# Kernel optimization log

Hardware: AMD Instinct MI355X
Metric: run time of the kernel (lower is better)

The kernel has to match this reference:

```python
import jax, jax.numpy as jnp
import numpy as np

STDDEV = 0.1  # matches Regularizer(stddev=0.1)


def setup_inputs() -> dict:
    key = jax.random.key(0)
    k1, k2, k3, k4 = jax.random.split(key, 4)
    B, S, D = 2048, 256, 128  # batch, num_samples, n_input
    return {
        "x": jax.random.normal(k1, (B, D), dtype=jnp.float32),
        "noise": jax.random.normal(k2, (B, S, D), dtype=jnp.float32),
        "W": jax.random.normal(k3, (D, 1), dtype=jnp.float32) * 0.1,  # inner model weight
        "b": jax.random.normal(k4, (1,), dtype=jnp.float32),          # inner model bias
    }


def reference(x, noise, W, b):
    B, S, D = noise.shape
    # neighborhood: x repeated + Gaussian noise, plus constant column -> [B, S, D+1]
    xl_feat = x[:, None, :] + noise * STDDEV                      # [B, S, D]
    ones = jnp.ones((B, S, 1), dtype=x.dtype)
    xl = jnp.concatenate([xl_feat, ones], axis=-1)                # [B, S, D+1]

    # inner model (linear + sigmoid classifier) evaluated on the neighborhood
    y = jax.nn.sigmoid(xl_feat @ W + b)                           # [B, S, 1]

    # local least-squares fit: Beta = (X^T X)^{-1} X^T y, batched over B
    XtX = jnp.einsum('bsi,bsj->bij', xl, xl)                      # [B, D+1, D+1]
    Xty = jnp.einsum('bsi,bsk->bik', xl, y)                       # [B, D+1, 1]
    Beta = jnp.linalg.solve(XtX, Xty)                             # [B, D+1, 1]

    # linear predictions -> sigmoid -> BCE(target = model output)
    y_lin = jnp.einsum('bsi,bik->bsk', xl, Beta)                  # [B, S, 1]
    logp = jax.nn.log_sigmoid(y_lin)
    log1mp = jax.nn.log_sigmoid(-y_lin)
    bce = -(y * logp + (1.0 - y) * log1mp)                        # [B, S, 1]
    # mean over stacked per-sample BCE means == global mean (equal sizes)
    return jnp.mean(bce)
```

## Files before the change

kernel.cpp:

```cpp
#include <hip/hip_runtime.h>
#include <math.h>

#define NB 2048
#define NS 256
#define ND 128
#define NCOL 129
#define LDA 132
#define TS 32
#define XTP 40
#define BSTRIDE 132
#define STDDEV 0.1f

typedef __attribute__((ext_vector_type(8))) short bf16x8;
typedef __attribute__((ext_vector_type(4))) float f32x4;

__device__ inline unsigned short f32_to_bf16_rn(float f) {
  unsigned int u = __float_as_uint(f);
  unsigned int r = (u + 0x7FFFu + ((u >> 16) & 1u)) >> 16;
  return (unsigned short)r;
}
__device__ inline float bf16u_to_f32(unsigned short h) {
  return __uint_as_float(((unsigned int)h) << 16);
}
__device__ inline float rdlane(float v, int lane) {
// ... 37 lines not shown
  cornb = fmaf(-mb_, bc##c, cornb); \
  cornr = fmaf(-mb_, rh##c, cornr); \
  UPDS }

#define PUBROW(c) \
  *(float4*)&rbp[(c) * LDA + txc0] = make_float4(a##c##_0, a##c##_1, a##c##_2, a##c##_3); \
  *(float4*)&rbp[(c) * LDA + txc1] = make_float4(a##c##_4, a##c##_5, a##c##_6, a##c##_7);

#define TRAIL_C(c) { \
  const float4 o0_ = *(const float4*)&rbp[(c) * LDA + ty8]; \
  const float4 o1_ = *(const float4*)&rbp[(c) * LDA + ty8 + 4]; \
  const float4 c0_ = *(const float4*)&rbp[(c) * LDA + txc0]; \
  const float4 c1_ = *(const float4*)&rbp[(c) * LDA + txc1]; \
  const float pk_ = pd[(c)]; \
  const float m0 = o0_.x*pk_, m1 = o0_.y*pk_, m2 = o0_.z*pk_, m3 = o0_.w*pk_; \
  const float m4 = o1_.x*pk_, m5 = o1_.y*pk_, m6 = o1_.z*pk_, m7 = o1_.w*pk_; \
  const float rc0 = c0_.x, rc1 = c0_.y, rc2 = c0_.z, rc3 = c0_.w; \
  const float rc4 = c1_.x, rc5 = c1_.y, rc6 = c1_.z, rc7 = c1_.w; \
  FOR_ALL(ACC_UPD) \
  hr0 = fmaf(m0, rp[(c)], hr0); hr1 = fmaf(m1, rp[(c)], hr1); \
  hr2 = fmaf(m2, rp[(c)], hr2); hr3 = fmaf(m3, rp[(c)], hr3); \
  hr4 = fmaf(m4, rp[(c)], hr4); hr5 = fmaf(m5, rp[(c)], hr5); \
  hr6 = fmaf(m6, rp[(c)], hr6); hr7 = fmaf(m7, rp[(c)], hr7); \
  hb0 = fmaf(m0, bp[(c)], hb0); hb1 = fmaf(m1, bp[(c)], hb1); \
  hb2 = fmaf(m2, bp[(c)], hb2); hb3 = fmaf(m3, bp[(c)], hb3); \
  hb4 = fmaf(m4, bp[(c)], hb4); hb5 = fmaf(m5, bp[(c)], hb5); \
  hb6 = fmaf(m6, bp[(c)], hb6); hb7 = fmaf(m7, bp[(c)], hb7); }

#define PC_U(cc, J, SRC, bev) { const float u_ = rdlane(a##cc##_##J, SRC); \
  rh##cc = fmaf(-u_, bev, rh##cc); }
#define PC_S(c, UPDS) { be##c = rh##c * pd##c; UPDS }

#define PCT_ROW(i) const float ps##i = hi \
  ? fmaf(a##i##_4, be0, fmaf(a##i##_5, be1, fmaf(a##i##_6, be2, a##i##_7 * be3))) \
  : fmaf(a##i##_0, be0, fmaf(a##i##_1, be1, fmaf(a##i##_2, be2, a##i##_3 * be3)));

#define FOR_J(F) F(0) F(1) F(2) F(3) F(4) F(5) F(6) F(7)
#define CB_DECL(j) f32x4 cb0_##j = {0.f,0.f,0.f,0.f}; f32x4 cb1_##j = {0.f,0.f,0.f,0.f};

#define MF_J(j) { \
  const bf16x8 Bh = *(const bf16x8*)&XTh[(16*(j) + tx)*XTP + kq]; \
  const bf16x8 Bl = *(const bf16x8*)&XTl[(16*(j) + tx)*XTP + kq]; \
  cb0_##j = __builtin_amdgcn_mfma_f32_16x16x32_bf16(Ah0, Bh, cb0_##j, 0,0,0); \
  cb0_##j = __builtin_amdgcn_mfma_f32_16x16x32_bf16(Ah0, Bl, cb0_##j, 0,0,0); \
  cb0_##j = __builtin_amdgcn_mfma_f32_16x16x32_bf16(Al0, Bh, cb0_##j, 0,0,0); \
  cb1_##j = __builtin_amdgcn_mfma_f32_16x16x32_bf16(Ah1, Bh, cb1_##j, 0,0,0); \
  cb1_##j = __builtin_amdgcn_mfma_f32_16x16x32_bf16(Ah1, Bl, cb1_##j, 0,0,0); \
  cb1_##j = __builtin_amdgcn_mfma_f32_16x16x32_bf16(Al1, Bh, cb1_##j, 0,0,0); }

#define TCONV(u, HV, LV, e) { \
  const float xf_ = sA[(sh + (u)) * LDA + d]; \
  const unsigned short hh_ = f32_to_bf16_rn(xf_); \
  const float hf_ = bf16u_to_f32(hh_); \
  const unsigned short ll_ = f32_to_bf16_rn(xf_ - hf_); \
  HV[e] = (short)hh_; LV[e] = (short)ll_; }

#define STAGE_IT(it, nv) { \
  const int idx_ = t + (it) * 256; \
  const int s_ = idx_ >> 5, d4_ = idx_ & 31; \
  const float4 xq_ = *(const float4*)&xv[d4_ * 4]; \
  float4 xl_; \
  xl_.x = xq_.x + STDDEV * nv.x; \
  xl_.y = xq_.y + STDDEV * nv.y; \
  xl_.z = xq_.z + STDDEV * nv.z; \
  xl_.w = xq_.w + STDDEV * nv.w; \
  *(float4*)&sA[s_ * LDA + d4_ * 4] = xl_; }

#define BW_BJ(b, j) \
  myband[(16*(b) + q4 + 0)*132 + 16*(j) + tx] = cb##b##_##j[0]; \
  myband[(16*(b) + q4 + 1)*132 + 16*(j) + tx] = cb##b##_##j[1]; \
  myband[(16*(b) + q4 + 2)*132 + 16*(j) + tx] = cb##b##_##j[2]; \
  myband[(16*(b) + q4 + 3)*132 + 16*(j) + tx] = cb##b##_##j[3];
#define BW_ALL \
  BW_BJ(0,0) BW_BJ(0,1) BW_BJ(0,2) BW_BJ(0,3) BW_BJ(0,4) BW_BJ(0,5) BW_BJ(0,6) BW_BJ(0,7) \
  BW_BJ(1,0) BW_BJ(1,1) BW_BJ(1,2) BW_BJ(1,3) BW_BJ(1,4) BW_BJ(1,5) BW_BJ(1,6) BW_BJ(1,7)
#define BR_ROW(i) { \
  const float4 lo_ = *(const float4*)&myband[(q8 + (i))*132 + txc0]; \
  const float4 hi_ = *(const float4*)&myband[(q8 + (i))*132 + txc1]; \
  a##i##_0 = lo_.x; a##i##_1 = lo_.y; a##i##_2 = lo_.z; a##i##_3 = lo_.w; \
  a##i##_4 = hi_.x; a##i##_5 = hi_.y; a##i##_6 = hi_.z; a##i##_7 = hi_.w; }
#define BR_ALL \
  BR_ROW(0) BR_ROW(1) BR_ROW(2) BR_ROW(3) BR_ROW(4) BR_ROW(5) BR_ROW(6) BR_ROW(7)

__global__ __launch_bounds__(256, 2)
void k_fit(const float* __restrict__ x, const float* __restrict__ noise,
           const float* __restrict__ W, const float* __restrict__ bptr,
           float* __restrict__ Beta) {
  __shared__ __align__(16) float region0[9344];
  __shared__ __align__(16) float pdiag[NCOL + 3];
  __shared__ __align__(16) float bcol[NCOL + 3];
  __shared__ __align__(16) float rhs[NCOL + 3];
  __shared__ __align__(16) float betaL[NCOL + 3];
  __shared__ __align__(16) float yt[TS];
  __shared__ __align__(16) float Wl[128];
  __shared__ __align__(16) float xv[128];

  float* sA = region0;
  unsigned short* XTh = (unsigned short*)(region0 + 4224);
  unsigned short* XTl = (unsigned short*)(region0 + 4224 + 2560);
  float* band = region0;
  float* rbuf = region0;
  float* sp0  = region0 + 2112;
  float* sp1  = region0 + 2240;

  const int t  = threadIdx.x;
  const int b  = blockIdx.x;
  const int tx = t & 15;
  const int ty = t >> 4;
  const int wv = t >> 6;
  const int txc0 = tx * 4;
  const int txc1 = 64 + tx * 4;
  const int ty8 = ty * 8;
  const int q4 = 4 * (ty & 3);
  const int q8 = 8 * (ty & 3);
  const int kq = 8 * (ty & 3);
  const float bscal = bptr[0];

  if (t < 128) { Wl[t] = W[t]; xv[t] = x[(size_t)b * ND + t]; }

  FOR_J(CB_DECL)
  float col_acc = 0.f, xty_acc = 0.f;

  const float* nbase = noise + (size_t)b * (NS * ND);

  float4 nv0, nv1, nv2, nv3;
  {
    const float4* src = (const float4*)nbase;
    nv0 = src[t]; nv1 = src[t + 256]; nv2 = src[t + 512]; nv3 = src[t + 768];
  }

  for (int s0 = 0; s0 < NS; s0 += TS) {
    __syncthreads();
    {
      STAGE_IT(0, nv0) STAGE_IT(1, nv1) STAGE_IT(2, nv2) STAGE_IT(3, nv3)
      if (t < TS) sA[t * LDA + ND] = 1.0f;
    }
    if (s0 + TS < NS) {
      const float4* src = (const float4*)(nbase + (size_t)(s0 + TS) * ND);
      nv0 = src[t]; nv1 = src[t + 256]; nv2 = src[t + 512]; nv3 = src[t + 768];
    }
    __syncthreads();
    {
      const int d = t >> 1;
      const int sh = (t & 1) * 16;
      bf16x8 h0, h1, l0, l1;
      TCONV(0,h0,l0,0) TCONV(1,h0,l0,1) TCONV(2,h0,l0,2) TCONV(3,h0,l0,3)
      TCONV(4,h0,l0,4) TCONV(5,h0,l0,5) TCONV(6,h0,l0,6) TCONV(7,h0,l0,7)
      TCONV(8,h1,l1,0) TCONV(9,h1,l1,1) TCONV(10,h1,l1,2) TCONV(11,h1,l1,3)
      TCONV(12,h1,l1,4) TCONV(13,h1,l1,5) TCONV(14,h1,l1,6) TCONV(15,h1,l1,7)
      *(bf16x8*)&XTh[d * XTP + sh]     = h0;
      *(bf16x8*)&XTh[d * XTP + sh + 8] = h1;
      *(bf16x8*)&XTl[d * XTP + sh]     = l0;
      *(bf16x8*)&XTl[d * XTP + sh + 8] = l1;
    }
    {
      int sl = t >> 3, p = t & 7;
      float acw = 0.f;
#pragma unroll
      for (int d = 0; d < 4; ++d) {
        float4 a = *(const float4*)&sA[sl * LDA + p * 16 + d * 4];
        float4 w = *(const float4*)&Wl[p * 16 + d * 4];
        acw += a.x * w.x + a.y * w.y + a.z * w.z + a.w * w.w;
      }
      acw += __shfl_xor(acw, 1);
      acw += __shfl_xor(acw, 2);
      acw += __shfl_xor(acw, 4);
      if (p == 0) yt[sl] = 1.f / (1.f + expf(-(acw + bscal)));
    }
    __syncthreads();
    if (t < NCOL) {
      for (int s = 0; s < TS; ++s) {
        float v = sA[s * LDA + t];
        col_acc += v;
        xty_acc += yt[s] * v;
      }
    }
    {
      const bf16x8 Ah0 = *(const bf16x8*)&XTh[(32*wv + tx)*XTP + kq];
      const bf16x8 Al0 = *(const bf16x8*)&XTl[(32*wv + tx)*XTP + kq];
      const bf16x8 Ah1 = *(const bf16x8*)&XTh[(32*wv + 16 + tx)*XTP + kq];
      const bf16x8 Al1 = *(const bf16x8*)&XTl[(32*wv + 16 + tx)*XTP + kq];
      MF_J(0) MF_J(1) MF_J(2) MF_J(3) MF_J(4) MF_J(5) MF_J(6) MF_J(7)
    }
  }
  if (t < NCOL) { bcol[t] = col_acc; rhs[t] = xty_acc; }
  __syncthreads();

  FOR_ALL(ACC_DECL)
  {
    float* myband = band + (wv & 1) * 4224;
    if (wv < 2) {
      BW_ALL
      asm volatile("s_waitcnt lgkmcnt(0)" ::: "memory");
      BR_ALL
      asm volatile("s_waitcnt lgkmcnt(0)" ::: "memory");
    }
    __syncthreads();
    if (wv >= 2) {
      BW_ALL
      asm volatile("s_waitcnt lgkmcnt(0)" ::: "memory");
      BR_ALL
      asm volatile("s_waitcnt lgkmcnt(0)" ::: "memory");
    }
    __syncthreads();
  }

#pragma unroll 1
  for (int p = 0; p < 16; ++p) {
    const int p8 = p * 8;
    const int ol = (p < 8) ? (p << 1) : ((p - 8) << 1);
    float* rbp = &rbuf[(p & 1) * (8 * LDA)];
    if (ty == p) {
      asm volatile("s_waitcnt lgkmcnt(0)" ::: "memory");
      const float4 rq0 = *(const float4*)&rhs[p8];
      const float4 rq1 = *(const float4*)&rhs[p8 + 4];
      const float4 bq0 = *(const float4*)&bcol[p8];
      const float4 bq1 = *(const float4*)&bcol[p8 + 4];
      float rh0 = rq0.x, rh1 = rq0.y, rh2 = rq0.z, rh3 = rq0.w;
      float rh4 = rq1.x, rh5 = rq1.y, rh6 = rq1.z, rh7 = rq1.w;
      float bc0 = bq0.x, bc1 = bq0.y, bc2 = bq0.z, bc3 = bq0.w;
      float bc4 = bq1.x, bc5 = bq1.y, bc6 = bq1.z, bc7 = bq1.w;
      float cornr = rhs[ND], cornb = bcol[ND];
      const int lsrc0 = ((p & 3) << 4) + ol;
      const int lsrc1 = lsrc0 + 1;
      if (p < 8) {
        PF_STEP(0, 0,1,2,3, PF_U(0,1) PF_U(0,2) PF_U(0,3) PF_U(0,4) PF_U(0,5) PF_U(0,6) PF_U(0,7))
        PF_STEP(1, 0,1,2,3, PF_U(1,2) PF_U(1,3) PF_U(1,4) PF_U(1,5) PF_U(1,6) PF_U(1,7))
        PF_STEP(2, 0,1,2,3, PF_U(2,3) PF_U(2,4) PF_U(2,5) PF_U(2,6) PF_U(2,7))
        PF_STEP(3, 0,1,2,3, PF_U(3,4) PF_U(3,5) PF_U(3,6) PF_U(3,7))
        PF_STEP(4, 0,1,2,3, PF_U(4,5) PF_U(4,6) PF_U(4,7))
        PF_STEP(5, 0,1,2,3, PF_U(5,6) PF_U(5,7))
        PF_STEP(6, 0,1,2,3, PF_U(6,7))
        PF_STEP(7, 0,1,2,3, )
      } else {
        PF_STEP(0, 4,5,6,7, PF_U(0,1) PF_U(0,2) PF_U(0,3) PF_U(0,4) PF_U(0,5) PF_U(0,6) PF_U(0,7))
        PF_STEP(1, 4,5,6,7, PF_U(1,2) PF_U(1,3) PF_U(1,4) PF_U(1,5) PF_U(1,6) PF_U(1,7))
        PF_STEP(2, 4,5,6,7, PF_U(2,3) PF_U(2,4) PF_U(2,5) PF_U(2,6) PF_U(2,7))
        PF_STEP(3, 4,5,6,7, PF_U(3,4) PF_U(3,5) PF_U(3,6) PF_U(3,7))
        PF_STEP(4, 4,5,6,7, PF_U(4,5) PF_U(4,6) PF_U(4,7))
        PF_STEP(5, 4,5,6,7, PF_U(5,6) PF_U(5,7))
        PF_STEP(6, 4,5,6,7, PF_U(6,7))
        PF_STEP(7, 4,5,6,7, )
      }
      PUBROW(0) PUBROW(1) PUBROW(2) PUBROW(3)
      PUBROW(4) PUBROW(5) PUBROW(6) PUBROW(7)
      if (tx == 0) {
        *(float4*)&rhs[p8]     = make_float4(rh0, rh1, rh2, rh3);
        *(float4*)&rhs[p8 + 4] = make_float4(rh4, rh5, rh6, rh7);
      }
      if (tx == 1) {
        *(float4*)&bcol[p8]     = make_float4(bc0, bc1, bc2, bc3);
        *(float4*)&bcol[p8 + 4] = make_float4(bc4, bc5, bc6, bc7);
      }
      if (tx == 2) { rhs[ND] = cornr; bcol[ND] = cornb; }
    }
    __syncthreads();
    if (ty > p) {
      const float4 d0_ = *(const float4*)&pdiag[p8];
      const float4 d1_ = *(const float4*)&pdiag[p8 + 4];
      const float4 rq0_ = *(const float4*)&rhs[p8];
      const float4 rq1_ = *(const float4*)&rhs[p8 + 4];
      const float4 bq0_ = *(const float4*)&bcol[p8];
      const float4 bq1_ = *(const float4*)&bcol[p8 + 4];
      const float pd[8] = {d0_.x, d0_.y, d0_.z, d0_.w, d1_.x, d1_.y, d1_.z, d1_.w};
      const float rp[8] = {rq0_.x, rq0_.y, rq0_.z, rq0_.w, rq1_.x, rq1_.y, rq1_.z, rq1_.w};
      const float bp[8] = {bq0_.x, bq0_.y, bq0_.z, bq0_.w, bq1_.x, bq1_.y, bq1_.z, bq1_.w};
      float hr0 = 0.f, hr1 = 0.f, hr2 = 0.f, hr3 = 0.f;
      float hr4 = 0.f, hr5 = 0.f, hr6 = 0.f, hr7 = 0.f;
      float hb0 = 0.f, hb1 = 0.f, hb2 = 0.f, hb3 = 0.f;
      float hb4 = 0.f, hb5 = 0.f, hb6 = 0.f, hb7 = 0.f;
      TRAIL_C(0) TRAIL_C(1) TRAIL_C(2) TRAIL_C(3)
      TRAIL_C(4) TRAIL_C(5) TRAIL_C(6) TRAIL_C(7)
      if (tx == 0) {
        float4 h0 = *(float4*)&rhs[ty8]; float4 h1 = *(float4*)&rhs[ty8 + 4];
        h0.x -= hr0; h0.y -= hr1; h0.z -= hr2; h0.w -= hr3;
        h1.x -= hr4; h1.y -= hr5; h1.z -= hr6; h1.w -= hr7;
        *(float4*)&rhs[ty8] = h0; *(float4*)&rhs[ty8 + 4] = h1;
      }
      if (tx == 1) {
        float4 h0 = *(float4*)&bcol[ty8]; float4 h1 = *(float4*)&bcol[ty8 + 4];
        h0.x -= hb0; h0.y -= hb1; h0.z -= hb2; h0.w -= hb3;
        h1.x -= hb4; h1.y -= hb5; h1.z -= hb6; h1.w -= hb7;
        *(float4*)&bcol[ty8] = h0; *(float4*)&bcol[ty8 + 4] = h1;
      }
    }
  }
  __syncthreads();

  if (t == 0) betaL[ND] = rhs[ND] / bcol[ND];
  if (t < ND) { sp0[t] = 0.f; sp1[t] = 0.f; }
  __syncthreads();
  if (t < ND) rhs[t] = fmaf(-bcol[t], betaL[ND], rhs[t]);
  __syncthreads();
#pragma unroll 1
  for (int p = 15; p >= 0; --p) {
    const int p8 = p * 8;
    const bool hi = (p >= 8);
    const int ol = hi ? ((p - 8) << 1) : (p << 1);
    const int txo0 = ol, txo1 = ol + 1;
    if (ty == p) {
      asm volatile("s_waitcnt lgkmcnt(0)" ::: "memory");
      const float4 rq0 = *(const float4*)&rhs[p8];
      const float4 rq1 = *(const float4*)&rhs[p8 + 4];
      const float4 sq0 = *(const float4*)&sp0[p8];
      const float4 sq1 = *(const float4*)&sp0[p8 + 4];
      const float4 uq0 = *(const float4*)&sp1[p8];
      const float4 uq1 = *(const float4*)&sp1[p8 + 4];
      const float4 dq0 = *(const float4*)&pdiag[p8];
      const float4 dq1 = *(const float4*)&pdiag[p8 + 4];
      float rh0 = rq0.x - sq0.x - uq0.x, rh1 = rq0.y - sq0.y - uq0.y;
      float rh2 = rq0.z - sq0.z - uq0.z, rh3 = rq0.w - sq0.w - uq0.w;
      float rh4 = rq1.x - sq1.x - uq1.x, rh5 = rq1.y - sq1.y - uq1.y;
      float rh6 = rq1.z - sq1.z - uq1.z, rh7 = rq1.w - sq1.w - uq1.w;
      const float pd0 = dq0.x, pd1 = dq0.y, pd2 = dq0.z, pd3 = dq0.w;
      const float pd4 = dq1.x, pd5 = dq1.y, pd6 = dq1.z, pd7 = dq1.w;
      const int lsrc0 = ((p & 3) << 4) + ol;
      const int lsrc1 = lsrc0 + 1;
      float be0, be1, be2, be3, be4, be5, be6, be7;
      if (p < 8) {
        PC_S(7, PC_U(0,3,lsrc1,be7) PC_U(1,3,lsrc1,be7) PC_U(2,3,lsrc1,be7) PC_U(3,3,lsrc1,be7) PC_U(4,3,lsrc1,be7) PC_U(5,3,lsrc1,be7) PC_U(6,3,lsrc1,be7))
        PC_S(6, PC_U(0,2,lsrc1,be6) PC_U(1,2,lsrc1,be6) PC_U(2,2,lsrc1,be6) PC_U(3,2,lsrc1,be6) PC_U(4,2,lsrc1,be6) PC_U(5,2,lsrc1,be6))
        PC_S(5, PC_U(0,1,lsrc1,be5) PC_U(1,1,lsrc1,be5) PC_U(2,1,lsrc1,be5) PC_U(3,1,lsrc1,be5) PC_U(4,1,lsrc1,be5))
        PC_S(4, PC_U(0,0,lsrc1,be4) PC_U(1,0,lsrc1,be4) PC_U(2,0,lsrc1,be4) PC_U(3,0,lsrc1,be4))
        PC_S(3, PC_U(0,3,lsrc0,be3) PC_U(1,3,lsrc0,be3) PC_U(2,3,lsrc0,be3))
        PC_S(2, PC_U(0,2,lsrc0,be2) PC_U(1,2,lsrc0,be2))
        PC_S(1, PC_U(0,1,lsrc0,be1))
        PC_S(0, )
      } else {
        PC_S(7, PC_U(0,7,lsrc1,be7) PC_U(1,7,lsrc1,be7) PC_U(2,7,lsrc1,be7) PC_U(3,7,lsrc1,be7) PC_U(4,7,lsrc1,be7) PC_U(5,7,lsrc1,be7) PC_U(6,7,lsrc1,be7))
        PC_S(6, PC_U(0,6,lsrc1,be6) PC_U(1,6,lsrc1,be6) PC_U(2,6,lsrc1,be6) PC_U(3,6,lsrc1,be6) PC_U(4,6,lsrc1,be6) PC_U(5,6,lsrc1,be6))
        PC_S(5, PC_U(0,5,lsrc1,be5) PC_U(1,5,lsrc1,be5) PC_U(2,5,lsrc1,be5) PC_U(3,5,lsrc1,be5) PC_U(4,5,lsrc1,be5))
        PC_S(4, PC_U(0,4,lsrc1,be4) PC_U(1,4,lsrc1,be4) PC_U(2,4,lsrc1,be4) PC_U(3,4,lsrc1,be4))
        PC_S(3, PC_U(0,7,lsrc0,be3) PC_U(1,7,lsrc0,be3) PC_U(2,7,lsrc0,be3))
        PC_S(2, PC_U(0,6,lsrc0,be2) PC_U(1,6,lsrc0,be2))
        PC_S(1, PC_U(0,5,lsrc0,be1))
        PC_S(0, )
      }
      if (tx == 0) {
        *(float4*)&betaL[p8]     = make_float4(be0, be1, be2, be3);
        *(float4*)&betaL[p8 + 4] = make_float4(be4, be5, be6, be7);
      }
    }
    __syncthreads();
    if (ty < p && (tx == txo0 || tx == txo1)) {
      const bool second = (tx == txo1);
      const float4 beq = *(const float4*)&betaL[p8 + (second ? 4 : 0)];
      float* spd = second ? sp1 : sp0;
      const float be0 = beq.x, be1 = beq.y, be2 = beq.z, be3 = beq.w;
      PCT_ROW(0) PCT_ROW(1) PCT_ROW(2) PCT_ROW(3)
      PCT_ROW(4) PCT_ROW(5) PCT_ROW(6) PCT_ROW(7)
      float4 h0 = *(float4*)&spd[ty8]; float4 h1 = *(float4*)&spd[ty8 + 4];
      h0.x += ps0; h0.y += ps1; h0.z += ps2; h0.w += ps3;
      h1.x += ps4; h1.y += ps5; h1.z += ps6; h1.w += ps7;
      *(float4*)&spd[ty8] = h0; *(float4*)&spd[ty8 + 4] = h1;
    }
    __syncthreads();
  }
  if (t < NCOL) Beta[(size_t)b * BSTRIDE + t] = betaL[t];
}

__device__ inline float logsig(float v) {
  if (v >= 0.f) return -log1pf(expf(-v));
  return v - log1pf(expf(v));
}

__global__ __launch_bounds__(256)
void k_bce(const float* __restrict__ x, const float* __restrict__ noise,
           const float* __restrict__ W, const float* __restrict__ bptr,
           const float* __restrict__ Beta, float* __restrict__ partial) {
  const int t    = threadIdx.x;
  const int lane = t & 31;
  const int grp  = t >> 5;
  const int bb   = blockIdx.x >> 2;
  const size_t sbase = (size_t)blockIdx.x * 64;
  __shared__ float saw[64], sab[64];

  const float4 w4 = *((const float4*)W + lane);
  const float4 x4 = *((const float4*)x + (size_t)bb * 32 + lane);
  const float4 p4 = *((const float4*)(Beta + (size_t)bb * BSTRIDE) + lane);

  for (int it = 0; it < 8; ++it) {
    const size_t idx = sbase + grp * 8 + it;
    float4 n4 = *((const float4*)noise + idx * 32 + lane);
    float4 xl;
    xl.x = x4.x + STDDEV * n4.x;
    xl.y = x4.y + STDDEV * n4.y;
    xl.z = x4.z + STDDEV * n4.z;
    xl.w = x4.w + STDDEV * n4.w;
    float aw = xl.x * w4.x + xl.y * w4.y + xl.z * w4.z + xl.w * w4.w;
    float ab = xl.x * p4.x + xl.y * p4.y + xl.z * p4.z + xl.w * p4.w;
#pragma unroll
    for (int off = 16; off >= 1; off >>= 1) {
      aw += __shfl_xor(aw, off);
      ab += __shfl_xor(ab, off);
    }
    if (lane == 0) { saw[grp * 8 + it] = aw; sab[grp * 8 + it] = ab; }
  }
  __syncthreads();
  if (t < 64) {
    const float bscal = bptr[0];
    const float beta128 = Beta[(size_t)bb * BSTRIDE + 128];
    const float y    = 1.f / (1.f + expf(-(saw[t] + bscal)));
    const float ylin = sab[t] + beta128;
    float v = -(y * logsig(ylin) + (1.f - y) * logsig(-ylin));
#pragma unroll
    for (int off = 32; off >= 1; off >>= 1) v += __shfl_xor(v, off);
    if (t == 0) partial[blockIdx.x] = v;
  }
}

__global__ void k_final(const float* __restrict__ partial, float* __restrict__ out,
                        int n, float inv) {
  __shared__ float red[256];
  float s = 0.f;
  for (int i = threadIdx.x; i < n; i += 256) s += partial[i];
  red[threadIdx.x] = s;
  __syncthreads();
  for (int k = 128; k > 0; k >>= 1) {
    if (threadIdx.x < k) red[threadIdx.x] += red[threadIdx.x + k];
    __syncthreads();
  }
  if (threadIdx.x == 0) out[0] = red[0] * inv;
}

extern "C" void kernel_launch(void* const* d_in, const int* in_sizes, int n_in,
                              void* d_out, int out_size, void* d_ws, size_t ws_size,
                              hipStream_t stream) {
  const float* x     = (const float*)d_in[0];
  const float* noise = (const float*)d_in[1];
  const float* W     = (const float*)d_in[2];
  const float* bptr  = (const float*)d_in[3];
  float* out = (float*)d_out;

  float* Beta = (float*)d_ws;
  const size_t beta_bytes = (size_t)NB * BSTRIDE * sizeof(float);
  float* partial = (float*)((char*)d_ws + ((beta_bytes + 255) & ~(size_t)255));

  const int nblk2 = (NB * NS) / 64;

  k_fit<<<NB, 256, 0, stream>>>(x, noise, W, bptr, Beta);
  k_bce<<<nblk2, 256, 0, stream>>>(x, noise, W, bptr, Beta, partial);
  k_final<<<1, 256, 0, stream>>>(partial, out, nblk2, 1.0f / (float)(NB * NS));
}
```

Measured before the change: 388.3 us.

## Split fused fit kernel into form and solve kernels via global XtX buffer

The monolithic per-batch fit kernel is split into k_form, which accumulates XtX with MFMA and writes it plus column sums and Xty to global workspace, and k_solve, which reloads them and runs the blocked elimination and back-substitution. Each kernel asks for 3 blocks per CU instead of 2, so the memory-bound formation phase and the sync-heavy solve phase no longer share one resource footprint. The cost is an extra round trip of about 128 MB for the XtX matrices through global memory and one more launch. The old fused kernel stays as a fallback when the workspace is too small.

```diff
diff --git a/kernel.cpp b/kernel.cpp
--- a/kernel.cpp
+++ b/kernel.cpp
@@ -143,15 +143,238 @@
 #define BR_ALL \
   BR_ROW(0) BR_ROW(1) BR_ROW(2) BR_ROW(3) BR_ROW(4) BR_ROW(5) BR_ROW(6) BR_ROW(7)
 
-__global__ __launch_bounds__(256, 2)
-void k_fit(const float* __restrict__ x, const float* __restrict__ noise,
-           const float* __restrict__ W, const float* __restrict__ bptr,
-           float* __restrict__ Beta) {
+#define PHASE_A_BODY \
+  for (int s0 = 0; s0 < NS; s0 += TS) { \
+    __syncthreads(); \
+    { STAGE_IT(0, nv0) STAGE_IT(1, nv1) STAGE_IT(2, nv2) STAGE_IT(3, nv3) \
+      if (t < TS) sA[t * LDA + ND] = 1.0f; } \
+    if (s0 + TS < NS) { \
+      const float4* src = (const float4*)(nbase + (size_t)(s0 + TS) * ND); \
+      nv0 = src[t]; nv1 = src[t + 256]; nv2 = src[t + 512]; nv3 = src[t + 768]; \
+    } \
+    __syncthreads(); \
+    { const int d = t >> 1; \
+      const int sh = (t & 1) * 16; \
+      bf16x8 h0, h1, l0, l1; \
+      TCONV(0,h0,l0,0) TCONV(1,h0,l0,1) TCONV(2,h0,l0,2) TCONV(3,h0,l0,3) \
+      TCONV(4,h0,l0,4) TCONV(5,h0,l0,5) TCONV(6,h0,l0,6) TCONV(7,h0,l0,7) \
+      TCONV(8,h1,l1,0) TCONV(9,h1,l1,1) TCONV(10,h1,l1,2) TCONV(11,h1,l1,3) \
+      TCONV(12,h1,l1,4) TCONV(13,h1,l1,5) TCONV(14,h1,l1,6) TCONV(15,h1,l1,7) \
+      *(bf16x8*)&XTh[d * XTP + sh]     = h0; \
+      *(bf16x8*)&XTh[d * XTP + sh + 8] = h1; \
+      *(bf16x8*)&XTl[d * XTP + sh]     = l0; \
+      *(bf16x8*)&XTl[d * XTP + sh + 8] = l1; } \
+    { int sl = t >> 3, p = t & 7; \
+      float acw = 0.f; \
+      _Pragma("unroll") \
+      for (int d = 0; d < 4; ++d) { \
+        float4 a = *(const float4*)&sA[sl * LDA + p * 16 + d * 4]; \
+        float4 w = *(const float4*)&Wl[p * 16 + d * 4]; \
+        acw += a.x * w.x + a.y * w.y + a.z * w.z + a.w * w.w; \
+      } \
+      acw += __shfl_xor(acw, 1); \
+      acw += __shfl_xor(acw, 2); \
+      acw += __shfl_xor(acw, 4); \
+      if (p == 0) yt[sl] = 1.f / (1.f + expf(-(acw + bscal))); } \
+    __syncthreads(); \
+    if (t < NCOL) { \
+      for (int s = 0; s < TS; ++s) { \
+        float v = sA[s * LDA + t]; \
+        col_acc += v; \
+        xty_acc += yt[s] * v; \
+      } } \
+    { const bf16x8 Ah0 = *(const bf16x8*)&XTh[(32*wv + tx)*XTP + kq]; \
+      const bf16x8 Al0 = *(const bf16x8*)&XTl[(32*wv + tx)*XTP + kq]; \
+      const bf16x8 Ah1 = *(const bf16x8*)&XTh[(32*wv + 16 + tx)*XTP + kq]; \
+      const bf16x8 Al1 = *(const bf16x8*)&XTl[(32*wv + 16 + tx)*XTP + kq]; \
+      MF_J(0) MF_J(1) MF_J(2) MF_J(3) MF_J(4) MF_J(5) MF_J(6) MF_J(7) } \
+  }
+
+#define BRIDGE_BODY \
+  { float* myband = band + (wv & 1) * 4224; \
+    if (wv < 2) { \
+      BW_ALL \
+      asm volatile("s_waitcnt lgkmcnt(0)" ::: "memory"); \
+      BR_ALL \
+      asm volatile("s_waitcnt lgkmcnt(0)" ::: "memory"); \
+    } \
+    __syncthreads(); \
+    if (wv >= 2) { \
+      BW_ALL \
+      asm volatile("s_waitcnt lgkmcnt(0)" ::: "memory"); \
+      BR_ALL \
+      asm volatile("s_waitcnt lgkmcnt(0)" ::: "memory"); \
+    } \
+    __syncthreads(); }
+
+#define PHASE_B_BODY \
+  _Pragma("unroll 1") \
+  for (int p = 0; p < 16; ++p) { \
+    const int p8 = p * 8; \
+    const int ol = (p < 8) ? (p << 1) : ((p - 8) << 1); \
+    float* rbp = &rbuf[(p & 1) * (8 * LDA)]; \
+    if (ty == p) { \
+      asm volatile("s_waitcnt lgkmcnt(0)" ::: "memory"); \
+      const float4 rq0 = *(const float4*)&rhs[p8]; \
+      const float4 rq1 = *(const float4*)&rhs[p8 + 4]; \
+      const float4 bq0 = *(const float4*)&bcol[p8]; \
+      const float4 bq1 = *(const float4*)&bcol[p8 + 4]; \
+      float rh0 = rq0.x, rh1 = rq0.y, rh2 = rq0.z, rh3 = rq0.w; \
+      float rh4 = rq1.x, rh5 = rq1.y, rh6 = rq1.z, rh7 = rq1.w; \
+      float bc0 = bq0.x, bc1 = bq0.y, bc2 = bq0.z, bc3 = bq0.w; \
+      float bc4 = bq1.x, bc5 = bq1.y, bc6 = bq1.z, bc7 = bq1.w; \
+      float cornr = rhs[ND], cornb = bcol[ND]; \
+      const int lsrc0 = ((p & 3) << 4) + ol; \
+      const int lsrc1 = lsrc0 + 1; \
+      if (p < 8) { \
+        PF_STEP(0, 0,1,2,3, PF_U(0,1) PF_U(0,2) PF_U(0,3) PF_U(0,4) PF_U(0,5) PF_U(0,6) PF_U(0,7)) \
+        PF_STEP(1, 0,1,2,3, PF_U(1,2) PF_U(1,3) PF_U(1,4) PF_U(1,5) PF_U(1,6) PF_U(1,7)) \
+        PF_STEP(2, 0,1,2,3, PF_U(2,3) PF_U(2,4) PF_U(2,5) PF_U(2,6) PF_U(2,7)) \
+        PF_STEP(3, 0,1,2,3, PF_U(3,4) PF_U(3,5) PF_U(3,6) PF_U(3,7)) \
+        PF_STEP(4, 0,1,2,3, PF_U(4,5) PF_U(4,6) PF_U(4,7)) \
+        PF_STEP(5, 0,1,2,3, PF_U(5,6) PF_U(5,7)) \
+        PF_STEP(6, 0,1,2,3, PF_U(6,7)) \
+        PF_STEP(7, 0,1,2,3, ) \
+      } else { \
+        PF_STEP(0, 4,5,6,7, PF_U(0,1) PF_U(0,2) PF_U(0,3) PF_U(0,4) PF_U(0,5) PF_U(0,6) PF_U(0,7)) \
+        PF_STEP(1, 4,5,6,7, PF_U(1,2) PF_U(1,3) PF_U(1,4) PF_U(1,5) PF_U(1,6) PF_U(1,7)) \
+        PF_STEP(2, 4,5,6,7, PF_U(2,3) PF_U(2,4) PF_U(2,5) PF_U(2,6) PF_U(2,7)) \
+        PF_STEP(3, 4,5,6,7, PF_U(3,4) PF_U(3,5) PF_U(3,6) PF_U(3,7)) \
+        PF_STEP(4, 4,5,6,7, PF_U(4,5) PF_U(4,6) PF_U(4,7)) \
+        PF_STEP(5, 4,5,6,7, PF_U(5,6) PF_U(5,7)) \
+        PF_STEP(6, 4,5,6,7, PF_U(6,7)) \
+        PF_STEP(7, 4,5,6,7, ) \
+      } \
+      PUBROW(0) PUBROW(1) PUBROW(2) PUBROW(3) \
+      PUBROW(4) PUBROW(5) PUBROW(6) PUBROW(7) \
+      if (tx == 0) { \
+        *(float4*)&rhs[p8]     = make_float4(rh0, rh1, rh2, rh3); \
+        *(float4*)&rhs[p8 + 4] = make_float4(rh4, rh5, rh6, rh7); \
+      } \
+      if (tx == 1) { \
+        *(float4*)&bcol[p8]     = make_float4(bc0, bc1, bc2, bc3); \
+        *(float4*)&bcol[p8 + 4] = make_float4(bc4, bc5, bc6, bc7); \
+      } \
+      if (tx == 2) { rhs[ND] = cornr; bcol[ND] = cornb; } \
+    } \
+    __syncthreads(); \
+    if (ty > p) { \
+      const float4 d0_ = *(const float4*)&pdiag[p8]; \
+      const float4 d1_ = *(const float4*)&pdiag[p8 + 4]; \
+      const float4 rq0_ = *(const float4*)&rhs[p8]; \
+      const float4 rq1_ = *(const float4*)&rhs[p8 + 4]; \
+      const float4 bq0_ = *(const float4*)&bcol[p8]; \
+      const float4 bq1_ = *(const float4*)&bcol[p8 + 4]; \
+      const float pd[8] = {d0_.x, d0_.y, d0_.z, d0_.w, d1_.x, d1_.y, d1_.z, d1_.w}; \
+      const float rp[8] = {rq0_.x, rq0_.y, rq0_.z, rq0_.w, rq1_.x, rq1_.y, rq1_.z, rq1_.w}; \
+      const float bp[8] = {bq0_.x, bq0_.y, bq0_.z, bq0_.w, bq1_.x, bq1_.y, bq1_.z, bq1_.w}; \
+      float hr0 = 0.f, hr1 = 0.f, hr2 = 0.f, hr3 = 0.f; \
+      float hr4 = 0.f, hr5 = 0.f, hr6 = 0.f, hr7 = 0.f; \
+      float hb0 = 0.f, hb1 = 0.f, hb2 = 0.f, hb3 = 0.f; \
+      float hb4 = 0.f, hb5 = 0.f, hb6 = 0.f, hb7 = 0.f; \
+      TRAIL_C(0) TRAIL_C(1) TRAIL_C(2) TRAIL_C(3) \
+      TRAIL_C(4) TRAIL_C(5) TRAIL_C(6) TRAIL_C(7) \
+      if (tx == 0) { \
+        float4 h0 = *(float4*)&rhs[ty8]; float4 h1 = *(float4*)&rhs[ty8 + 4]; \
+        h0.x -= hr0; h0.y -= hr1; h0.z -= hr2; h0.w -= hr3; \
+        h1.x -= hr4; h1.y -= hr5; h1.z -= hr6; h1.w -= hr7; \
+        *(float4*)&rhs[ty8] = h0; *(float4*)&rhs[ty8 + 4] = h1; \
+      } \
+      if (tx == 1) { \
+        float4 h0 = *(float4*)&bcol[ty8]; float4 h1 = *(float4*)&bcol[ty8 + 4]; \
+        h0.x -= hb0; h0.y -= hb1; h0.z -= hb2; h0.w -= hb3; \
+        h1.x -= hb4; h1.y -= hb5; h1.z -= hb6; h1.w -= hb7; \
+        *(float4*)&bcol[ty8] = h0; *(float4*)&bcol[ty8 + 4] = h1; \
+      } \
+    } \
+  } \
+  __syncthreads();
+
+#define PHASE_C_BODY \
+  if (t == 0) betaL[ND] = rhs[ND] / bcol[ND]; \
+  if (t < ND) { sp0[t] = 0.f; sp1[t] = 0.f; } \
+  __syncthreads(); \
+  if (t < ND) rhs[t] = fmaf(-bcol[t], betaL[ND], rhs[t]); \
+  __syncthreads(); \
+  _Pragma("unroll 1") \
+  for (int p = 15; p >= 0; --p) { \
+    const int p8 = p * 8; \
+    const bool hi = (p >= 8); \
+    const int ol = hi ? ((p - 8) << 1) : (p << 1); \
+    const int txo0 = ol, txo1 = ol + 1; \
+    if (ty == p) { \
+      asm volatile("s_waitcnt lgkmcnt(0)" ::: "memory"); \
+      const float4 rq0 = *(const float4*)&rhs[p8]; \
+      const float4 rq1 = *(const float4*)&rhs[p8 + 4]; \
+      const float4 sq0 = *(const float4*)&sp0[p8]; \
+      const float4 sq1 = *(const float4*)&sp0[p8 + 4]; \
+      const float4 uq0 = *(const float4*)&sp1[p8]; \
+      const float4 uq1 = *(const float4*)&sp1[p8 + 4]; \
+      const float4 dq0 = *(const float4*)&pdiag[p8]; \
+      const float4 dq1 = *(const float4*)&pdiag[p8 + 4]; \
+      float rh0 = rq0.x - sq0.x - uq0.x, rh1 = rq0.y - sq0.y - uq0.y; \
+      float rh2 = rq0.z - sq0.z - uq0.z, rh3 = rq0.w - sq0.w - uq0.w; \
+      float rh4 = rq1.x - sq1.x - uq1.x, rh5 = rq1.y - sq1.y - uq1.y; \
+      float rh6 = rq1.z - sq1.z - uq1.z, rh7 = rq1.w - sq1.w - uq1.w; \
+      const float pd0 = dq0.x, pd1 = dq0.y, pd2 = dq0.z, pd3 = dq0.w; \
+      const float pd4 = dq1.x, pd5 = dq1.y, pd6 = dq1.z, pd7 = dq1.w; \
+      const int lsrc0 = ((p & 3) << 4) + ol; \
+      const int lsrc1 = lsrc0 + 1; \
+      float be0, be1, be2, be3, be4, be5, be6, be7; \
+      if (p < 8) { \
+        PC_S(7, PC_U(0,3,lsrc1,be7) PC_U(1,3,lsrc1,be7) PC_U(2,3,lsrc1,be7) PC_U(3,3,lsrc1,be7) PC_U(4,3,lsrc1,be7) PC_U(5,3,lsrc1,be7) PC_U(6,3,lsrc1,be7)) \
+        PC_S(6, PC_U(0,2,lsrc1,be6) PC_U(1,2,lsrc1,be6) PC_U(2,2,lsrc1,be6) PC_U(3,2,lsrc1,be6) PC_U(4,2,lsrc1,be6) PC_U(5,2,lsrc1,be6)) \
+        PC_S(5, PC_U(0,1,lsrc1,be5) PC_U(1,1,lsrc1,be5) PC_U(2,1,lsrc1,be5) PC_U(3,1,lsrc1,be5) PC_U(4,1,lsrc1,be5)) \
+        PC_S(4, PC_U(0,0,lsrc1,be4) PC_U(1,0,lsrc1,be4) PC_U(2,0,lsrc1,be4) PC_U(3,0,lsrc1,be4)) \
+        PC_S(3, PC_U(0,3,lsrc0,be3) PC_U(1,3,lsrc0,be3) PC_U(2,3,lsrc0,be3)) \
+        PC_S(2, PC_U(0,2,lsrc0,be2) PC_U(1,2,lsrc0,be2)) \
+        PC_S(1, PC_U(0,1,lsrc0,be1)) \
+        PC_S(0, ) \
+      } else { \
+        PC_S(7, PC_U(0,7,lsrc1,be7) PC_U(1,7,lsrc1,be7) PC_U(2,7,lsrc1,be7) PC_U(3,7,lsrc1,be7) PC_U(4,7,lsrc1,be7) PC_U(5,7,lsrc1,be7) PC_U(6,7,lsrc1,be7)) \
+        PC_S(6, PC_U(0,6,lsrc1,be6) PC_U(1,6,lsrc1,be6) PC_U(2,6,lsrc1,be6) PC_U(3,6,lsrc1,be6) PC_U(4,6,lsrc1,be6) PC_U(5,6,lsrc1,be6)) \
+        PC_S(5, PC_U(0,5,lsrc1,be5) PC_U(1,5,lsrc1,be5) PC_U(2,5,lsrc1,be5) PC_U(3,5,lsrc1,be5) PC_U(4,5,lsrc1,be5)) \
+        PC_S(4, PC_U(0,4,lsrc1,be4) PC_U(1,4,lsrc1,be4) PC_U(2,4,lsrc1,be4) PC_U(3,4,lsrc1,be4)) \
+        PC_S(3, PC_U(0,7,lsrc0,be3) PC_U(1,7,lsrc0,be3) PC_U(2,7,lsrc0,be3)) \
+        PC_S(2, PC_U(0,6,lsrc0,be2) PC_U(1,6,lsrc0,be2)) \
+        PC_S(1, PC_U(0,5,lsrc0,be1)) \
+        PC_S(0, ) \
+      } \
+      if (tx == 0) { \
+        *(float4*)&betaL[p8]     = make_float4(be0, be1, be2, be3); \
+        *(float4*)&betaL[p8 + 4] = make_float4(be4, be5, be6, be7); \
+      } \
+    } \
+    __syncthreads(); \
+    if (ty < p && (tx == txo0 || tx == txo1)) { \
+      const bool second = (tx == txo1); \
+      const float4 beq = *(const float4*)&betaL[p8 + (second ? 4 : 0)]; \
+      float* spd = second ? sp1 : sp0; \
+      const float be0 = beq.x, be1 = beq.y, be2 = beq.z, be3 = beq.w; \
+      PCT_ROW(0) PCT_ROW(1) PCT_ROW(2) PCT_ROW(3) \
+      PCT_ROW(4) PCT_ROW(5) PCT_ROW(6) PCT_ROW(7) \
+      float4 h0 = *(float4*)&spd[ty8]; float4 h1 = *(float4*)&spd[ty8 + 4]; \
+      h0.x += ps0; h0.y += ps1; h0.z += ps2; h0.w += ps3; \
+      h1.x += ps4; h1.y += ps5; h1.z += ps6; h1.w += ps7; \
+      *(float4*)&spd[ty8] = h0; *(float4*)&spd[ty8 + 4] = h1; \
+    } \
+    __syncthreads(); \
+  }
+
+#define ST_ROW(i) { \
+  *(float4*)&Xg[(ty8 + (i))*128 + txc0] = make_float4(a##i##_0, a##i##_1, a##i##_2, a##i##_3); \
+  *(float4*)&Xg[(ty8 + (i))*128 + txc1] = make_float4(a##i##_4, a##i##_5, a##i##_6, a##i##_7); }
+#define LD_ROW(i) { \
+  const float4 lo_ = *(const float4*)&Xg[(ty8 + (i))*128 + txc0]; \
+  const float4 hi_ = *(const float4*)&Xg[(ty8 + (i))*128 + txc1]; \
+  a##i##_0 = lo_.x; a##i##_1 = lo_.y; a##i##_2 = lo_.z; a##i##_3 = lo_.w; \
+  a##i##_4 = hi_.x; a##i##_5 = hi_.y; a##i##_6 = hi_.z; a##i##_7 = hi_.w; }
+
+__global__ __launch_bounds__(256, 3)
+void k_form(const float* __restrict__ x, const float* __restrict__ noise,
+            const float* __restrict__ W, const float* __restrict__ bptr,
+            float* __restrict__ brg, float* __restrict__ xtx) {
   __shared__ __align__(16) float region0[9344];
-  __shared__ __align__(16) float pdiag[NCOL + 3];
-  __shared__ __align__(16) float bcol[NCOL + 3];
-  __shared__ __align__(16) float rhs[NCOL + 3];
-  __shared__ __align__(16) float betaL[NCOL + 3];
   __shared__ __align__(16) float yt[TS];
   __shared__ __align__(16) float Wl[128];
   __shared__ __align__(16) float xv[128];
@@ -160,9 +383,6 @@
   unsigned short* XTh = (unsigned short*)(region0 + 4224);
   unsigned short* XTl = (unsigned short*)(region0 + 4224 + 2560);
   float* band = region0;
-  float* rbuf = region0;
-  float* sp0  = region0 + 2112;
-  float* sp1  = region0 + 2240;
 
   const int t  = threadIdx.x;
   const int b  = blockIdx.x;
@@ -183,240 +403,120 @@
   float col_acc = 0.f, xty_acc = 0.f;
 
   const float* nbase = noise + (size_t)b * (NS * ND);
-
   float4 nv0, nv1, nv2, nv3;
   {
     const float4* src = (const float4*)nbase;
     nv0 = src[t]; nv1 = src[t + 256]; nv2 = src[t + 512]; nv3 = src[t + 768];
   }
 
-  for (int s0 = 0; s0 < NS; s0 += TS) {
-    __syncthreads();
-    {
-      STAGE_IT(0, nv0) STAGE_IT(1, nv1) STAGE_IT(2, nv2) STAGE_IT(3, nv3)
-      if (t < TS) sA[t * LDA + ND] = 1.0f;
-    }
-    if (s0 + TS < NS) {
-      const float4* src = (const float4*)(nbase + (size_t)(s0 + TS) * ND);
-      nv0 = src[t]; nv1 = src[t + 256]; nv2 = src[t + 512]; nv3 = src[t + 768];
-    }
-    __syncthreads();
-    {
-      const int d = t >> 1;
-      const int sh = (t & 1) * 16;
-      bf16x8 h0, h1, l0, l1;
-      TCONV(0,h0,l0,0) TCONV(1,h0,l0,1) TCONV(2,h0,l0,2) TCONV(3,h0,l0,3)
-      TCONV(4,h0,l0,4) TCONV(5,h0,l0,5) TCONV(6,h0,l0,6) TCONV(7,h0,l0,7)
-      TCONV(8,h1,l1,0) TCONV(9,h1,l1,1) TCONV(10,h1,l1,2) TCONV(11,h1,l1,3)
-      TCONV(12,h1,l1,4) TCONV(13,h1,l1,5) TCONV(14,h1,l1,6) TCONV(15,h1,l1,7)
-      *(bf16x8*)&XTh[d * XTP + sh]     = h0;
-      *(bf16x8*)&XTh[d * XTP + sh + 8] = h1;
-      *(bf16x8*)&XTl[d * XTP + sh]     = l0;
-      *(bf16x8*)&XTl[d * XTP + sh + 8] = l1;
-    }
-    {
-      int sl = t >> 3, p = t & 7;
-      float acw = 0.f;
-#pragma unroll
-      for (int d = 0; d < 4; ++d) {
-        float4 a = *(const float4*)&sA[sl * LDA + p * 16 + d * 4];
-        float4 w = *(const float4*)&Wl[p * 16 + d * 4];
-        acw += a.x * w.x + a.y * w.y + a.z * w.z + a.w * w.w;
-      }
-      acw += __shfl_xor(acw, 1);
-      acw += __shfl_xor(acw, 2);
-      acw += __shfl_xor(acw, 4);
-      if (p == 0) yt[sl] = 1.f / (1.f + expf(-(acw + bscal)));
-    }
-    __syncthreads();
-    if (t < NCOL) {
-      for (int s = 0; s < TS; ++s) {
-        float v = sA[s * LDA + t];
-        col_acc += v;
-        xty_acc += yt[s] * v;
-      }
-    }
-    {
-      const bf16x8 Ah0 = *(const bf16x8*)&XTh[(32*wv + tx)*XTP + kq];
-      const bf16x8 Al0 = *(const bf16x8*)&XTl[(32*wv + tx)*XTP + kq];
-      const bf16x8 Ah1 = *(const bf16x8*)&XTh[(32*wv + 16 + tx)*XTP + kq];
-      const bf16x8 Al1 = *(const bf16x8*)&XTl[(32*wv + 16 + tx)*XTP + kq];
-      MF_J(0) MF_J(1) MF_J(2) MF_J(3) MF_J(4) MF_J(5) MF_J(6) MF_J(7)
-    }
-  }
+  PHASE_A_BODY
+
+  if (t < NCOL) {
+    float* br = brg + (size_t)b * 264;
+    br[t] = col_acc; br[132 + t] = xty_acc;
+  }
+  __syncthreads();
+
+  FOR_ALL(ACC_DECL)
+  BRIDGE_BODY
+
+  float* Xg = xtx + (size_t)b * 16384;
+  ST_ROW(0) ST_ROW(1) ST_ROW(2) ST_ROW(3)
+  ST_ROW(4) ST_ROW(5) ST_ROW(6) ST_ROW(7)
+}
+
+__global__ __launch_bounds__(256, 3)
+void k_solve(const float* __restrict__ brg, const float* __restrict__ xtx,
+             float* __restrict__ Beta) {
+  __shared__ __align__(16) float rbuf[2 * 8 * LDA];
+  __shared__ __align__(16) float pdiag[NCOL + 3];
+  __shared__ __align__(16) float bcol[NCOL + 3];
+  __shared__ __align__(16) float rhs[NCOL + 3];
+  __shared__ __align__(16) float betaL[NCOL + 3];
+  __shared__ __align__(16) float sp0[ND], sp1[ND];
+
+  const int t  = threadIdx.x;
+  const int b  = blockIdx.x;
+  const int tx = t & 15;
+  const int ty = t >> 4;
+  const int txc0 = tx * 4;
+  const int txc1 = 64 + tx * 4;
+  const int ty8 = ty * 8;
+
+  FOR_ALL(ACC_DECL)
+  {
+    const float* Xg = xtx + (size_t)b * 16384;
+    LD_ROW(0) LD_ROW(1) LD_ROW(2) LD_ROW(3)
+    LD_ROW(4) LD_ROW(5) LD_ROW(6) LD_ROW(7)
+  }
+  if (t < NCOL) {
+    const float* br = brg + (size_t)b * 264;
+    bcol[t] = br[t]; rhs[t] = br[132 + t];
+  }
+  __syncthreads();
+
+  PHASE_B_BODY
+  PHASE_C_BODY
+
+  if (t < NCOL) Beta[(size_t)b * BSTRIDE + t] = betaL[t];
+}
+
+__global__ __launch_bounds__(256, 2)
+void k_fit_mono(const float* __restrict__ x, const float* __restrict__ noise,
+                const float* __restrict__ W, const float* __restrict__ bptr,
+                float* __restrict__ Beta) {
+  __shared__ __align__(16) float region0[9344];
+  __shared__ __align__(16) float pdiag[NCOL + 3];
+  __shared__ __align__(16) float bcol[NCOL + 3];
+  __shared__ __align__(16) float rhs[NCOL + 3];
+  __shared__ __align__(16) float betaL[NCOL + 3];
+  __shared__ __align__(16) float yt[TS];
+  __shared__ __align__(16) float Wl[128];
+  __shared__ __align__(16) float xv[128];
+
+  float* sA = region0;
+  unsigned short* XTh = (unsigned short*)(region0 + 4224);
+  unsigned short* XTl = (unsigned short*)(region0 + 4224 + 2560);
+  float* band = region0;
+  float* rbuf = region0;
+  float* sp0  = region0 + 2112;
+  float* sp1  = region0 + 2240;
+
+  const int t  = threadIdx.x;
+  const int b  = blockIdx.x;
+  const int tx = t & 15;
+  const int ty = t >> 4;
+  const int wv = t >> 6;
+  const int txc0 = tx * 4;
+  const int txc1 = 64 + tx * 4;
+  const int ty8 = ty * 8;
+  const int q4 = 4 * (ty & 3);
+  const int q8 = 8 * (ty & 3);
+  const int kq = 8 * (ty & 3);
+  const float bscal = bptr[0];
+
+  if (t < 128) { Wl[t] = W[t]; xv[t] = x[(size_t)b * ND + t]; }
+
+  FOR_J(CB_DECL)
+  float col_acc = 0.f, xty_acc = 0.f;
+
+  const float* nbase = noise + (size_t)b * (NS * ND);
+  float4 nv0, nv1, nv2, nv3;
+  {
+    const float4* src = (const float4*)nbase;
+    nv0 = src[t]; nv1 = src[t + 256]; nv2 = src[t + 512]; nv3 = src[t + 768];
+  }
+
+  PHASE_A_BODY
+
   if (t < NCOL) { bcol[t] = col_acc; rhs[t] = xty_acc; }
   __syncthreads();
 
   FOR_ALL(ACC_DECL)
-  {
-    float* myband = band + (wv & 1) * 4224;
-    if (wv < 2) {
-      BW_ALL
-      asm volatile("s_waitcnt lgkmcnt(0)" ::: "memory");
-      BR_ALL
-      asm volatile("s_waitcnt lgkmcnt(0)" ::: "memory");
-    }
-    __syncthreads();
-    if (wv >= 2) {
-      BW_ALL
-      asm volatile("s_waitcnt lgkmcnt(0)" ::: "memory");
-      BR_ALL
-      asm volatile("s_waitcnt lgkmcnt(0)" ::: "memory");
-    }
-    __syncthreads();
-  }
-
-#pragma unroll 1
-  for (int p = 0; p < 16; ++p) {
-    const int p8 = p * 8;
-    const int ol = (p < 8) ? (p << 1) : ((p - 8) << 1);
-    float* rbp = &rbuf[(p & 1) * (8 * LDA)];
-    if (ty == p) {
-      asm volatile("s_waitcnt lgkmcnt(0)" ::: "memory");
-      const float4 rq0 = *(const float4*)&rhs[p8];
-      const float4 rq1 = *(const float4*)&rhs[p8 + 4];
-      const float4 bq0 = *(const float4*)&bcol[p8];
-      const float4 bq1 = *(const float4*)&bcol[p8 + 4];
-      float rh0 = rq0.x, rh1 = rq0.y, rh2 = rq0.z, rh3 = rq0.w;
-      float rh4 = rq1.x, rh5 = rq1.y, rh6 = rq1.z, rh7 = rq1.w;
-      float bc0 = bq0.x, bc1 = bq0.y, bc2 = bq0.z, bc3 = bq0.w;
-      float bc4 = bq1.x, bc5 = bq1.y, bc6 = bq1.z, bc7 = bq1.w;
-      float cornr = rhs[ND], cornb = bcol[ND];
-      const int lsrc0 = ((p & 3) << 4) + ol;
-      const int lsrc1 = lsrc0 + 1;
-      if (p < 8) {
-        PF_STEP(0, 0,1,2,3, PF_U(0,1) PF_U(0,2) PF_U(0,3) PF_U(0,4) PF_U(0,5) PF_U(0,6) PF_U(0,7))
-        PF_STEP(1, 0,1,2,3, PF_U(1,2) PF_U(1,3) PF_U(1,4) PF_U(1,5) PF_U(1,6) PF_U(1,7))
-        PF_STEP(2, 0,1,2,3, PF_U(2,3) PF_U(2,4) PF_U(2,5) PF_U(2,6) PF_U(2,7))
-        PF_STEP(3, 0,1,2,3, PF_U(3,4) PF_U(3,5) PF_U(3,6) PF_U(3,7))
-        PF_STEP(4, 0,1,2,3, PF_U(4,5) PF_U(4,6) PF_U(4,7))
-        PF_STEP(5, 0,1,2,3, PF_U(5,6) PF_U(5,7))
-        PF_STEP(6, 0,1,2,3, PF_U(6,7))
-        PF_STEP(7, 0,1,2,3, )
-      } else {
-        PF_STEP(0, 4,5,6,7, PF_U(0,1) PF_U(0,2) PF_U(0,3) PF_U(0,4) PF_U(0,5) PF_U(0,6) PF_U(0,7))
-        PF_STEP(1, 4,5,6,7, PF_U(1,2) PF_U(1,3) PF_U(1,4) PF_U(1,5) PF_U(1,6) PF_U(1,7))
-        PF_STEP(2, 4,5,6,7, PF_U(2,3) PF_U(2,4) PF_U(2,5) PF_U(2,6) PF_U(2,7))
-        PF_STEP(3, 4,5,6,7, PF_U(3,4) PF_U(3,5) PF_U(3,6) PF_U(3,7))
-        PF_STEP(4, 4,5,6,7, PF_U(4,5) PF_U(4,6) PF_U(4,7))
-        PF_STEP(5, 4,5,6,7, PF_U(5,6) PF_U(5,7))
-        PF_STEP(6, 4,5,6,7, PF_U(6,7))
-        PF_STEP(7, 4,5,6,7, )
-      }
-      PUBROW(0) PUBROW(1) PUBROW(2) PUBROW(3)
-      PUBROW(4) PUBROW(5) PUBROW(6) PUBROW(7)
-      if (tx == 0) {
-        *(float4*)&rhs[p8]     = make_float4(rh0, rh1, rh2, rh3);
-        *(float4*)&rhs[p8 + 4] = make_float4(rh4, rh5, rh6, rh7);
-      }
-      if (tx == 1) {
-        *(float4*)&bcol[p8]     = make_float4(bc0, bc1, bc2, bc3);
-        *(float4*)&bcol[p8 + 4] = make_float4(bc4, bc5, bc6, bc7);
-      }
-      if (tx == 2) { rhs[ND] = cornr; bcol[ND] = cornb; }
-    }
-    __syncthreads();
-    if (ty > p) {
-      const float4 d0_ = *(const float4*)&pdiag[p8];
-      const float4 d1_ = *(const float4*)&pdiag[p8 + 4];
-      const float4 rq0_ = *(const float4*)&rhs[p8];
-      const float4 rq1_ = *(const float4*)&rhs[p8 + 4];
-      const float4 bq0_ = *(const float4*)&bcol[p8];
-      const float4 bq1_ = *(const float4*)&bcol[p8 + 4];
-      const float pd[8] = {d0_.x, d0_.y, d0_.z, d0_.w, d1_.x, d1_.y, d1_.z, d1_.w};
-      const float rp[8] = {rq0_.x, rq0_.y, rq0_.z, rq0_.w, rq1_.x, rq1_.y, rq1_.z, rq1_.w};
-      const float bp[8] = {bq0_.x, bq0_.y, bq0_.z, bq0_.w, bq1_.x, bq1_.y, bq1_.z, bq1_.w};
-      float hr0 = 0.f, hr1 = 0.f, hr2 = 0.f, hr3 = 0.f;
-      float hr4 = 0.f, hr5 = 0.f, hr6 = 0.f, hr7 = 0.f;
-      float hb0 = 0.f, hb1 = 0.f, hb2 = 0.f, hb3 = 0.f;
-      float hb4 = 0.f, hb5 = 0.f, hb6 = 0.f, hb7 = 0.f;
-      TRAIL_C(0) TRAIL_C(1) TRAIL_C(2) TRAIL_C(3)
-      TRAIL_C(4) TRAIL_C(5) TRAIL_C(6) TRAIL_C(7)
-      if (tx == 0) {
-        float4 h0 = *(float4*)&rhs[ty8]; float4 h1 = *(float4*)&rhs[ty8 + 4];
-        h0.x -= hr0; h0.y -= hr1; h0.z -= hr2; h0.w -= hr3;
-        h1.x -= hr4; h1.y -= hr5; h1.z -= hr6; h1.w -= hr7;
-        *(float4*)&rhs[ty8] = h0; *(float4*)&rhs[ty8 + 4] = h1;
-      }
-      if (tx == 1) {
-        float4 h0 = *(float4*)&bcol[ty8]; float4 h1 = *(float4*)&bcol[ty8 + 4];
-        h0.x -= hb0; h0.y -= hb1; h0.z -= hb2; h0.w -= hb3;
-        h1.x -= hb4; h1.y -= hb5; h1.z -= hb6; h1.w -= hb7;
-        *(float4*)&bcol[ty8] = h0; *(float4*)&bcol[ty8 + 4] = h1;
-      }
-    }
-  }
-  __syncthreads();
-
-  if (t == 0) betaL[ND] = rhs[ND] / bcol[ND];
-  if (t < ND) { sp0[t] = 0.f; sp1[t] = 0.f; }
-  __syncthreads();
-  if (t < ND) rhs[t] = fmaf(-bcol[t], betaL[ND], rhs[t]);
-  __syncthreads();
-#pragma unroll 1
-  for (int p = 15; p >= 0; --p) {
-    const int p8 = p * 8;
-    const bool hi = (p >= 8);
-    const int ol = hi ? ((p - 8) << 1) : (p << 1);
-    const int txo0 = ol, txo1 = ol + 1;
-    if (ty == p) {
-      asm volatile("s_waitcnt lgkmcnt(0)" ::: "memory");
-      const float4 rq0 = *(const float4*)&rhs[p8];
-      const float4 rq1 = *(const float4*)&rhs[p8 + 4];
-      const float4 sq0 = *(const float4*)&sp0[p8];
-      const float4 sq1 = *(const float4*)&sp0[p8 + 4];
-      const float4 uq0 = *(const float4*)&sp1[p8];
-      const float4 uq1 = *(const float4*)&sp1[p8 + 4];
-      const float4 dq0 = *(const float4*)&pdiag[p8];
-      const float4 dq1 = *(const float4*)&pdiag[p8 + 4];
-      float rh0 = rq0.x - sq0.x - uq0.x, rh1 = rq0.y - sq0.y - uq0.y;
-      float rh2 = rq0.z - sq0.z - uq0.z, rh3 = rq0.w - sq0.w - uq0.w;
-      float rh4 = rq1.x - sq1.x - uq1.x, rh5 = rq1.y - sq1.y - uq1.y;
-      float rh6 = rq1.z - sq1.z - uq1.z, rh7 = rq1.w - sq1.w - uq1.w;
-      const float pd0 = dq0.x, pd1 = dq0.y, pd2 = dq0.z, pd3 = dq0.w;
-      const float pd4 = dq1.x, pd5 = dq1.y, pd6 = dq1.z, pd7 = dq1.w;
-      const int lsrc0 = ((p & 3) << 4) + ol;
-      const int lsrc1 = lsrc0 + 1;
-      float be0, be1, be2, be3, be4, be5, be6, be7;
-      if (p < 8) {
-        PC_S(7, PC_U(0,3,lsrc1,be7) PC_U(1,3,lsrc1,be7) PC_U(2,3,lsrc1,be7) PC_U(3,3,lsrc1,be7) PC_U(4,3,lsrc1,be7) PC_U(5,3,lsrc1,be7) PC_U(6,3,lsrc1,be7))
-        PC_S(6, PC_U(0,2,lsrc1,be6) PC_U(1,2,lsrc1,be6) PC_U(2,2,lsrc1,be6) PC_U(3,2,lsrc1,be6) PC_U(4,2,lsrc1,be6) PC_U(5,2,lsrc1,be6))
-        PC_S(5, PC_U(0,1,lsrc1,be5) PC_U(1,1,lsrc1,be5) PC_U(2,1,lsrc1,be5) PC_U(3,1,lsrc1,be5) PC_U(4,1,lsrc1,be5))
-        PC_S(4, PC_U(0,0,lsrc1,be4) PC_U(1,0,lsrc1,be4) PC_U(2,0,lsrc1,be4) PC_U(3,0,lsrc1,be4))
-        PC_S(3, PC_U(0,3,lsrc0,be3) PC_U(1,3,lsrc0,be3) PC_U(2,3,lsrc0,be3))
-        PC_S(2, PC_U(0,2,lsrc0,be2) PC_U(1,2,lsrc0,be2))
-        PC_S(1, PC_U(0,1,lsrc0,be1))
-        PC_S(0, )
-      } else {
-        PC_S(7, PC_U(0,7,lsrc1,be7) PC_U(1,7,lsrc1,be7) PC_U(2,7,lsrc1,be7) PC_U(3,7,lsrc1,be7) PC_U(4,7,lsrc1,be7) PC_U(5,7,lsrc1,be7) PC_U(6,7,lsrc1,be7))
-        PC_S(6, PC_U(0,6,lsrc1,be6) PC_U(1,6,lsrc1,be6) PC_U(2,6,lsrc1,be6) PC_U(3,6,lsrc1,be6) PC_U(4,6,lsrc1,be6) PC_U(5,6,lsrc1,be6))
-        PC_S(5, PC_U(0,5,lsrc1,be5) PC_U(1,5,lsrc1,be5) PC_U(2,5,lsrc1,be5) PC_U(3,5,lsrc1,be5) PC_U(4,5,lsrc1,be5))
-        PC_S(4, PC_U(0,4,lsrc1,be4) PC_U(1,4,lsrc1,be4) PC_U(2,4,lsrc1,be4) PC_U(3,4,lsrc1,be4))
-        PC_S(3, PC_U(0,7,lsrc0,be3) PC_U(1,7,lsrc0,be3) PC_U(2,7,lsrc0,be3))
-        PC_S(2, PC_U(0,6,lsrc0,be2) PC_U(1,6,lsrc0,be2))
-        PC_S(1, PC_U(0,5,lsrc0,be1))
-        PC_S(0, )
-      }
-      if (tx == 0) {
-        *(float4*)&betaL[p8]     = make_float4(be0, be1, be2, be3);
-        *(float4*)&betaL[p8 + 4] = make_float4(be4, be5, be6, be7);
-      }
-    }
-    __syncthreads();
-    if (ty < p && (tx == txo0 || tx == txo1)) {
-      const bool second = (tx == txo1);
-      const float4 beq = *(const float4*)&betaL[p8 + (second ? 4 : 0)];
-      float* spd = second ? sp1 : sp0;
-      const float be0 = beq.x, be1 = beq.y, be2 = beq.z, be3 = beq.w;
-      PCT_ROW(0) PCT_ROW(1) PCT_ROW(2) PCT_ROW(3)
-      PCT_ROW(4) PCT_ROW(5) PCT_ROW(6) PCT_ROW(7)
-      float4 h0 = *(float4*)&spd[ty8]; float4 h1 = *(float4*)&spd[ty8 + 4];
-      h0.x += ps0; h0.y += ps1; h0.z += ps2; h0.w += ps3;
-      h1.x += ps4; h1.y += ps5; h1.z += ps6; h1.w += ps7;
-      *(float4*)&spd[ty8] = h0; *(float4*)&spd[ty8 + 4] = h1;
-    }
-    __syncthreads();
-  }
+  BRIDGE_BODY
+  PHASE_B_BODY
+  PHASE_C_BODY
+
   if (t < NCOL) Beta[(size_t)b * BSTRIDE + t] = betaL[t];
 }
 
@@ -493,13 +593,26 @@
   const float* bptr  = (const float*)d_in[3];
   float* out = (float*)d_out;
 
-  float* Beta = (float*)d_ws;
-  const size_t beta_bytes = (size_t)NB * BSTRIDE * sizeof(float);
-  float* partial = (float*)((char*)d_ws + ((beta_bytes + 255) & ~(size_t)255));
+  char* wsc = (char*)d_ws;
+  size_t off = 0;
+  float* Beta = (float*)(wsc + off);
+  off = (off + (size_t)NB * BSTRIDE * 4 + 255) & ~(size_t)255;
+  float* partial = (float*)(wsc + off);
+  off = (off + 8192 * 4 + 255) & ~(size_t)255;
+  float* brg = (float*)(wsc + off);
+  off = (off + (size_t)NB * 264 * 4 + 255) & ~(size_t)255;
+  float* xtx = (float*)(wsc + off);
+  off += (size_t)NB * 16384 * 4;
+  const bool split = (ws_size >= off);
 
   const int nblk2 = (NB * NS) / 64;
 
-  k_fit<<<NB, 256, 0, stream>>>(x, noise, W, bptr, Beta);
+  if (split) {
+    k_form<<<NB, 256, 0, stream>>>(x, noise, W, bptr, brg, xtx);
+    k_solve<<<NB, 256, 0, stream>>>(brg, xtx, Beta);
+  } else {
+    k_fit_mono<<<NB, 256, 0, stream>>>(x, noise, W, bptr, Beta);
+  }
   k_bce<<<nblk2, 256, 0, stream>>>(x, noise, W, bptr, Beta, partial);
   k_final<<<1, 256, 0, stream>>>(partial, out, nblk2, 1.0f / (float)(NB * NS));
 }
```

New measurement: 742.8 us. +91.3%, slower.
